# Kernel tuning notes

Hardware: AMD Instinct MI355X
Metric: run time of the kernel (lower is better)

## Reference

```python
import jax, jax.numpy as jnp
import numpy as np

BOX = 32  # uniform ROI crop size (y1-y0 = x1-x0 = 32)


def setup_inputs() -> dict:
    key = jax.random.key(0)
    k1, k2, k3 = jax.random.split(key, 3)
    B, C, H, W = 8, 256, 200, 200
    N = 512
    feature_map = jax.random.normal(k1, (B, C, H, W), dtype=jnp.float32)
    boxes_yx = jax.random.randint(k2, (N, 2), 0, H - BOX, dtype=jnp.int32)  # top-left (y0, x0)
    assoc = jax.random.randint(k3, (N,), 0, B, dtype=jnp.int32)            # sample index per box
    return {"feature_map": feature_map, "boxes_yx": boxes_yx, "assoc": assoc}


def reference(feature_map, boxes_yx, assoc):
    # Faithful RoiCut: for each box i, crop feature_map[assoc[i], :, y0:y0+BOX, x0:x0+BOX].
    # clip_boxes=True -> clip box coords into the scene extent.
    B, C, H, W = feature_map.shape
    yx = jnp.clip(boxes_yx, 0, jnp.array([H - BOX, W - BOX], dtype=boxes_yx.dtype))

    def crop(a, yx_i):
        fm = feature_map[a]  # [C, H, W] gather of the associated sample
        return jax.lax.dynamic_slice(fm, (jnp.int32(0), yx_i[0], yx_i[1]), (C, BOX, BOX))

    box_features = jax.vmap(crop)(assoc, yx)  # [N, C, BOX, BOX]
    return box_features
```

## Files before the change

### kernel.cpp

```cpp
#include <hip/hip_runtime.h>


typedef float v4f __attribute__((ext_vector_type(4)));

constexpr int C_    = 256;
constexpr int H_    = 200;
constexpr int W_    = 200;
constexpr int BOX_  = 32;
constexpr int N_    = 512;
constexpr int B_    = 8;
constexpr int PLANE  = H_ * W_;
constexpr int PLANE4 = PLANE / 4;

__global__ __launch_bounds__(512) void sort_boxes_kernel(
    const int* __restrict__ boxes,
    const int* __restrict__ assoc,
    unsigned int* __restrict__ keys,
    int* __restrict__ starts)
{
    __shared__ unsigned int key[N_];
    int t = threadIdx.x;

    int y0 = boxes[2 * t];
    int x0 = boxes[2 * t + 1];
    y0 = min(max(y0, 0), H_ - BOX_);
    x0 = min(max(x0, 0), W_ - BOX_);
    unsigned int a = (unsigned int)assoc[t];
    key[t] = (a << 25) | ((unsigned int)y0 << 17) | ((unsigned int)x0 << 9) | (unsigned int)t;
    __syncthreads();

    for (int k = 2; k <= N_; k <<= 1) {
        for (int j = k >> 1; j > 0; j >>= 1) {
            int ixj = t ^ j;
            if (ixj > t) {
                unsigned int va = key[t], vb = key[ixj];
                bool asc = ((t & k) == 0);
                if ((va > vb) == asc) { key[t] = vb; key[ixj] = va; }
            }
            __syncthreads();
        }
    }

    unsigned int v = key[t];
    keys[t] = v;
    int at = (int)(v >> 25);
    int ap = (t == 0) ? -1 : (int)(key[t - 1] >> 25);
    for (int aa = ap + 1; aa <= at; ++aa) starts[aa] = t;
    if (t == N_ - 1) for (int aa = at + 1; aa <= B_; ++aa) starts[aa] = N_;
}

__global__ __launch_bounds__(1024) void roicut_kernel(
    const float* __restrict__ fm,
    const unsigned int* __restrict__ keys,
    const int* __restrict__ starts,
    float* __restrict__ out)
{
    extern __shared__ float lds[];

    int bid = blockIdx.x;
    int a = bid >> 8;
    int c = bid & 255;
    int t = threadIdx.x;

    const v4f* src = (const v4f*)(fm + (size_t)(a * C_ + c) * PLANE);
    v4f* l4 = (v4f*)lds;
    v4f r0 = src[t];
    v4f r1 = src[t + 1024];
    v4f r2 = src[t + 2048];
    v4f r3 = src[t + 3072];
    v4f r4 = src[t + 4096];
    v4f r5 = src[t + 5120];
    v4f r6 = src[t + 6144];
    v4f r7 = src[t + 7168];
    v4f r8 = src[t + 8192];
    bool tail = (t + 9216) < PLANE4;
    v4f r9;
    if (tail) r9 = src[t + 9216];
    l4[t]        = r0;
    l4[t + 1024] = r1;
    l4[t + 2048] = r2;
    l4[t + 3072] = r3;
    l4[t + 4096] = r4;
    l4[t + 5120] = r5;
    l4[t + 6144] = r6;
    l4[t + 7168] = r7;
    l4[t + 8192] = r8;
    if (tail) l4[t + 9216] = r9;
    __syncthreads();

    int b0 = starts[a], b1 = starts[a + 1];
    int sub = t >> 8;
    int q   = t & 255;
    int y   = q >> 3;
    int xg  = (q & 7) << 2;

    for (int b = b0; b < b1; b += 4) {
        int bb = b + sub;
        if (bb < b1) {
            unsigned int v = keys[bb];
            int y0 = (v >> 17) & 255;
            int x0 = (v >> 9) & 255;
            int i  = (int)(v & 511u);
            const float* p = lds + (y0 + y) * W_ + (x0 + xg);
            v4f vv;
            vv[0] = p[0];
            vv[1] = p[1];
            vv[2] = p[2];
            vv[3] = p[3];
            v4f* dst = (v4f*)(out + (((size_t)i << 18) + ((size_t)c << 10) + (size_t)(q << 2)));
            __builtin_nontemporal_store(vv, dst);
        }
    }
}

extern "C" void kernel_launch(void* const* d_in, const int* in_sizes, int n_in,
                              void* d_out, int out_size, void* d_ws, size_t ws_size,
                              hipStream_t stream) {
    const float* fm    = (const float*)d_in[0];
    const int*   boxes = (const int*)d_in[1];
    const int*   assoc = (const int*)d_in[2];
    float*       out   = (float*)d_out;

    unsigned int* keys   = (unsigned int*)d_ws;
    int*          starts = (int*)d_ws + N_;

    (void)hipFuncSetAttribute((const void*)roicut_kernel,
                              hipFuncAttributeMaxDynamicSharedMemorySize,
                              PLANE * (int)sizeof(float));

    sort_boxes_kernel<<<1, N_, 0, stream>>>(boxes, assoc, keys, starts);

    int grid = B_ * C_;
    roicut_kernel<<<grid, 1024, PLANE * sizeof(float), stream>>>(fm, keys, starts, out);
}
```

Baseline: 173.4 us.

## Split each feature plane across two blocks to halve LDS footprint

```diff
diff --git a/kernel.cpp b/kernel.cpp
--- a/kernel.cpp
+++ b/kernel.cpp
@@ -3,14 +3,16 @@
 
 typedef float v4f __attribute__((ext_vector_type(4)));
 
-constexpr int C_    = 256;
-constexpr int H_    = 200;
-constexpr int W_    = 200;
-constexpr int BOX_  = 32;
-constexpr int N_    = 512;
-constexpr int B_    = 8;
+constexpr int C_     = 256;
+constexpr int H_     = 200;
+constexpr int W_     = 200;
+constexpr int BOX_   = 32;
+constexpr int N_     = 512;
+constexpr int B_     = 8;
 constexpr int PLANE  = H_ * W_;
-constexpr int PLANE4 = PLANE / 4;
+constexpr int HROWS  = 100;
+constexpr int HLDS   = HROWS * W_;
+constexpr int HLDS4  = HLDS / 4;
 
 __global__ __launch_bounds__(512) void sort_boxes_kernel(
     const int* __restrict__ boxes,
@@ -49,7 +51,7 @@
     if (t == N_ - 1) for (int aa = at + 1; aa <= B_; ++aa) starts[aa] = N_;
 }
 
-__global__ __launch_bounds__(1024) void roicut_kernel(
+__global__ __launch_bounds__(1024, 8) void roicut_kernel(
     const float* __restrict__ fm,
     const unsigned int* __restrict__ keys,
     const int* __restrict__ starts,
@@ -58,34 +60,25 @@
     extern __shared__ float lds[];
 
     int bid = blockIdx.x;
-    int a = bid >> 8;
-    int c = bid & 255;
+    int h = bid & 1;
+    int c = (bid >> 1) & 255;
+    int a = bid >> 9;
     int t = threadIdx.x;
 
-    const v4f* src = (const v4f*)(fm + (size_t)(a * C_ + c) * PLANE);
+    const v4f* src = (const v4f*)(fm + (size_t)(a * C_ + c) * PLANE) + h * HLDS4;
     v4f* l4 = (v4f*)lds;
     v4f r0 = src[t];
     v4f r1 = src[t + 1024];
     v4f r2 = src[t + 2048];
     v4f r3 = src[t + 3072];
-    v4f r4 = src[t + 4096];
-    v4f r5 = src[t + 5120];
-    v4f r6 = src[t + 6144];
-    v4f r7 = src[t + 7168];
-    v4f r8 = src[t + 8192];
-    bool tail = (t + 9216) < PLANE4;
-    v4f r9;
-    if (tail) r9 = src[t + 9216];
+    bool tail = t < (HLDS4 - 4096);
+    v4f r4;
+    if (tail) r4 = src[t + 4096];
     l4[t]        = r0;
     l4[t + 1024] = r1;
     l4[t + 2048] = r2;
     l4[t + 3072] = r3;
-    l4[t + 4096] = r4;
-    l4[t + 5120] = r5;
-    l4[t + 6144] = r6;
-    l4[t + 7168] = r7;
-    l4[t + 8192] = r8;
-    if (tail) l4[t + 9216] = r9;
+    if (tail) l4[t + 4096] = r4;
     __syncthreads();
 
     int b0 = starts[a], b1 = starts[a + 1];
@@ -93,6 +86,7 @@
     int q   = t & 255;
     int y   = q >> 3;
     int xg  = (q & 7) << 2;
+    int hbase = h * HROWS;
 
     for (int b = b0; b < b1; b += 4) {
         int bb = b + sub;
@@ -101,14 +95,17 @@
             int y0 = (v >> 17) & 255;
             int x0 = (v >> 9) & 255;
             int i  = (int)(v & 511u);
-            const float* p = lds + (y0 + y) * W_ + (x0 + xg);
-            v4f vv;
-            vv[0] = p[0];
-            vv[1] = p[1];
-            vv[2] = p[2];
-            vv[3] = p[3];
-            v4f* dst = (v4f*)(out + (((size_t)i << 18) + ((size_t)c << 10) + (size_t)(q << 2)));
-            __builtin_nontemporal_store(vv, dst);
+            int ly = y0 + y - hbase;
+            if (ly >= 0 && ly < HROWS) {
+                const float* p = lds + ly * W_ + (x0 + xg);
+                v4f vv;
+                vv[0] = p[0];
+                vv[1] = p[1];
+                vv[2] = p[2];
+                vv[3] = p[3];
+                v4f* dst = (v4f*)(out + (((size_t)i << 18) + ((size_t)c << 10) + (size_t)(q << 2)));
+                __builtin_nontemporal_store(vv, dst);
+            }
         }
     }
 }
@@ -126,10 +123,10 @@
 
     (void)hipFuncSetAttribute((const void*)roicut_kernel,
                               hipFuncAttributeMaxDynamicSharedMemorySize,
-                              PLANE * (int)sizeof(float));
+                              HLDS * (int)sizeof(float));
 
     sort_boxes_kernel<<<1, N_, 0, stream>>>(boxes, assoc, keys, starts);
 
-    int grid = B_ * C_;
-    roicut_kernel<<<grid, 1024, PLANE * sizeof(float), stream>>>(fm, keys, starts, out);
+    int grid = B_ * C_ * 2;
+    roicut_kernel<<<grid, 1024, HLDS * sizeof(float), stream>>>(fm, keys, starts, out);
 }
```

After: 172.5 us. No clear change (-0.5%).

## Read crops directly from global memory and bin boxes by sample and row band

Applied to the files above, without the earlier changes.

```diff
diff --git a/kernel.cpp b/kernel.cpp
--- a/kernel.cpp
+++ b/kernel.cpp
@@ -9,107 +9,84 @@
 constexpr int BOX_  = 32;
 constexpr int N_    = 512;
 constexpr int B_    = 8;
-constexpr int PLANE  = H_ * W_;
-constexpr int PLANE4 = PLANE / 4;
+constexpr int PLANE = H_ * W_;
+constexpr int YB    = 8;
+constexpr int NYB   = (H_ + YB - 1) / YB;
+constexpr int NBIN  = B_ * NYB;
+constexpr int NBINP = 256;
 
-__global__ __launch_bounds__(512) void sort_boxes_kernel(
+__global__ __launch_bounds__(512) void group_boxes_kernel(
     const int* __restrict__ boxes,
     const int* __restrict__ assoc,
     unsigned int* __restrict__ keys,
     int* __restrict__ starts)
 {
-    __shared__ unsigned int key[N_];
+    __shared__ int cnt[NBINP];
+    __shared__ int scan[NBINP];
+    __shared__ int baseS[NBINP];
     int t = threadIdx.x;
+
+    if (t < NBINP) cnt[t] = 0;
+    __syncthreads();
 
     int y0 = boxes[2 * t];
     int x0 = boxes[2 * t + 1];
     y0 = min(max(y0, 0), H_ - BOX_);
     x0 = min(max(x0, 0), W_ - BOX_);
-    unsigned int a = (unsigned int)assoc[t];
-    key[t] = (a << 25) | ((unsigned int)y0 << 17) | ((unsigned int)x0 << 9) | (unsigned int)t;
+    int a = assoc[t];
+    int bin = a * NYB + y0 / YB;
+    unsigned int key = ((unsigned int)y0 << 17) | ((unsigned int)x0 << 9) | (unsigned int)t;
+    int pos = atomicAdd(&cnt[bin], 1);
     __syncthreads();
 
-    for (int k = 2; k <= N_; k <<= 1) {
-        for (int j = k >> 1; j > 0; j >>= 1) {
-            int ixj = t ^ j;
-            if (ixj > t) {
-                unsigned int va = key[t], vb = key[ixj];
-                bool asc = ((t & k) == 0);
-                if ((va > vb) == asc) { key[t] = vb; key[ixj] = va; }
-            }
-            __syncthreads();
-        }
+    if (t < NBINP) scan[t] = cnt[t];
+    __syncthreads();
+    for (int d = 1; d < NBINP; d <<= 1) {
+        int v = 0;
+        if (t < NBINP && t >= d) v = scan[t - d];
+        __syncthreads();
+        if (t < NBINP) scan[t] += v;
+        __syncthreads();
     }
+    if (t < NBINP) baseS[t] = scan[t] - cnt[t];
+    __syncthreads();
 
-    unsigned int v = key[t];
-    keys[t] = v;
-    int at = (int)(v >> 25);
-    int ap = (t == 0) ? -1 : (int)(key[t - 1] >> 25);
-    for (int aa = ap + 1; aa <= at; ++aa) starts[aa] = t;
-    if (t == N_ - 1) for (int aa = at + 1; aa <= B_; ++aa) starts[aa] = N_;
+    keys[baseS[bin] + pos] = key;
+    if (t <= B_) starts[t] = (t == B_) ? N_ : baseS[t * NYB];
 }
 
-__global__ __launch_bounds__(1024) void roicut_kernel(
+__global__ __launch_bounds__(1024, 8) void roicut_kernel(
     const float* __restrict__ fm,
     const unsigned int* __restrict__ keys,
     const int* __restrict__ starts,
     float* __restrict__ out)
 {
-    extern __shared__ float lds[];
-
     int bid = blockIdx.x;
+    int c = bid & 255;
     int a = bid >> 8;
-    int c = bid & 255;
     int t = threadIdx.x;
 
-    const v4f* src = (const v4f*)(fm + (size_t)(a * C_ + c) * PLANE);
-    v4f* l4 = (v4f*)lds;
-    v4f r0 = src[t];
-    v4f r1 = src[t + 1024];
-    v4f r2 = src[t + 2048];
-    v4f r3 = src[t + 3072];
-    v4f r4 = src[t + 4096];
-    v4f r5 = src[t + 5120];
-    v4f r6 = src[t + 6144];
-    v4f r7 = src[t + 7168];
-    v4f r8 = src[t + 8192];
-    bool tail = (t + 9216) < PLANE4;
-    v4f r9;
-    if (tail) r9 = src[t + 9216];
-    l4[t]        = r0;
-    l4[t + 1024] = r1;
-    l4[t + 2048] = r2;
-    l4[t + 3072] = r3;
-    l4[t + 4096] = r4;
-    l4[t + 5120] = r5;
-    l4[t + 6144] = r6;
-    l4[t + 7168] = r7;
-    l4[t + 8192] = r8;
-    if (tail) l4[t + 9216] = r9;
-    __syncthreads();
-
-    int b0 = starts[a], b1 = starts[a + 1];
+    int b0  = starts[a], b1 = starts[a + 1];
     int sub = t >> 8;
     int q   = t & 255;
     int y   = q >> 3;
     int xg  = (q & 7) << 2;
 
-    for (int b = b0; b < b1; b += 4) {
-        int bb = b + sub;
-        if (bb < b1) {
-            unsigned int v = keys[bb];
-            int y0 = (v >> 17) & 255;
-            int x0 = (v >> 9) & 255;
-            int i  = (int)(v & 511u);
-            const float* p = lds + (y0 + y) * W_ + (x0 + xg);
-            v4f vv;
-            vv[0] = p[0];
-            vv[1] = p[1];
-            vv[2] = p[2];
-            vv[3] = p[3];
-            v4f* dst = (v4f*)(out + (((size_t)i << 18) + ((size_t)c << 10) + (size_t)(q << 2)));
-            __builtin_nontemporal_store(vv, dst);
-        }
+    const float* plane = fm + (size_t)(a * C_ + c) * PLANE;
+
+    for (int b = b0 + sub; b < b1; b += 4) {
+        unsigned int v = keys[b];
+        int y0 = (v >> 17) & 255;
+        int x0 = (v >> 9) & 255;
+        int i  = (int)(v & 511u);
+        const float* p = plane + (y0 + y) * W_ + (x0 + xg);
+        v4f vv;
+        vv[0] = p[0];
+        vv[1] = p[1];
+        vv[2] = p[2];
+        vv[3] = p[3];
+        v4f* dst = (v4f*)(out + (((size_t)i << 18) + ((size_t)c << 10) + (size_t)(q << 2)));
+        __builtin_nontemporal_store(vv, dst);
     }
 }
 
@@ -124,12 +101,8 @@
     unsigned int* keys   = (unsigned int*)d_ws;
     int*          starts = (int*)d_ws + N_;
 
-    (void)hipFuncSetAttribute((const void*)roicut_kernel,
-                              hipFuncAttributeMaxDynamicSharedMemorySize,
-                              PLANE * (int)sizeof(float));
-
-    sort_boxes_kernel<<<1, N_, 0, stream>>>(boxes, assoc, keys, starts);
+    group_boxes_kernel<<<1, N_, 0, stream>>>(boxes, assoc, keys, starts);
 
     int grid = B_ * C_;
-    roicut_kernel<<<grid, 1024, PLANE * sizeof(float), stream>>>(fm, keys, starts, out);
+    roicut_kernel<<<grid, 1024, 0, stream>>>(fm, keys, starts, out);
 }
```

Result: slower. 199.0 us (+14.8%).
